# Performance work log

Hardware: AMD Instinct MI355X
Metric: run time of the kernel (lower is better)

Reference implementation:

```python
import jax, jax.numpy as jnp
import numpy as np


def conv3d(x, w, b):
    # x: [B,C,D,H,W], w: [O,I,3,3,3], padding=1, stride=1
    y = jax.lax.conv_general_dilated(
        x, w, window_strides=(1, 1, 1), padding=[(1, 1)] * 3,
        dimension_numbers=("NCDHW", "OIDHW", "NCDHW"))
    return y + b[None, :, None, None, None]


def trilinear_sample(x, cd, ch, cw):
    # x: [B,C,D,H,W]; cd/ch/cw: [B,K,D,H,W] float sampling coords.
    # Zero padding outside the volume (invalid corners masked to 0).
    B, C, D, H, W = x.shape
    d0 = jnp.floor(cd); h0 = jnp.floor(ch); w0 = jnp.floor(cw)
    fd, fh, fw = cd - d0, ch - h0, cw - w0
    d0 = d0.astype(jnp.int32); h0 = h0.astype(jnp.int32); w0 = w0.astype(jnp.int32)
    gather = jax.vmap(lambda xb, z, y, xx: xb[:, z, y, xx])  # -> [B,C,K,D,H,W]
    out = jnp.zeros((B, C) + cd.shape[1:], x.dtype)
    for dz in (0, 1):
        wz = fd if dz else 1.0 - fd
        zi = d0 + dz
        for dy in (0, 1):
            wy = fh if dy else 1.0 - fh
            yi = h0 + dy
            for dx in (0, 1):
                wx = fw if dx else 1.0 - fw
                xi = w0 + dx
                valid = ((zi >= 0) & (zi < D) & (yi >= 0) & (yi < H)
                         & (xi >= 0) & (xi < W)).astype(x.dtype)
                v = gather(x, jnp.clip(zi, 0, D - 1), jnp.clip(yi, 0, H - 1),
                           jnp.clip(xi, 0, W - 1))
                out = out + (wz * wy * wx * valid)[:, None] * v
    return out


def deform_conv3d(x, offsets, mask, w, b):
    # Modulated deformable 3D conv (DCNv2-style), kernel 3x3x3, pad 1, stride 1.
    # offsets: [B,81,D,H,W] = 27 taps x (dd,dh,dw); mask: [B,27,D,H,W].
    B, C, D, H, W = x.shape
    K = 27
    off = offsets.reshape(B, K, 3, D, H, W)
    kd, kh, kw = jnp.meshgrid(jnp.arange(3), jnp.arange(3), jnp.arange(3), indexing="ij")
    tap_d = (kd.reshape(-1) - 1).astype(x.dtype)[None, :, None, None, None]
    tap_h = (kh.reshape(-1) - 1).astype(x.dtype)[None, :, None, None, None]
    tap_w = (kw.reshape(-1) - 1).astype(x.dtype)[None, :, None, None, None]
    gd = jnp.arange(D, dtype=x.dtype)[None, None, :, None, None]
    gh = jnp.arange(H, dtype=x.dtype)[None, None, None, :, None]
    gw = jnp.arange(W, dtype=x.dtype)[None, None, None, None, :]
    cd = gd + tap_d + off[:, :, 0]
    ch = gh + tap_h + off[:, :, 1]
    cw = gw + tap_w + off[:, :, 2]
    sampled = trilinear_sample(x, cd, ch, cw) * mask[:, None]  # [B,C,K,D,H,W]
    out = jnp.einsum("bckdhw,ock->bodhw", sampled, w.reshape(w.shape[0], C, K))
    return out + b[None, :, None, None, None]


def mdconv3d(x, ow, ob, w, b):
    # MDConv3d: internal offset/mask predictor + modulated deformable conv.
    d = conv3d(x, ow, ob)
    offsets, mask = d[:, :81], jax.nn.sigmoid(d[:, 81:])
    return deform_conv3d(x, offsets, mask, w, b)


def forward(x, ow1, ob1, w1, b1, ow2, ob2, w2, b2, ow3, ob3, w3, b3,
            defo_w, defo_b, c3d_w, c3d_b):
    h = jax.nn.relu(mdconv3d(x, ow1, ob1, w1, b1))
    h = jax.nn.relu(mdconv3d(h, ow2, ob2, w2, b2))
    h = jax.nn.relu(mdconv3d(h, ow3, ob3, w3, b3))
    d = conv3d(h, defo_w, defo_b)
    offsets, alpha = d[:, :81], jax.nn.sigmoid(d[:, 81:])
    return deform_conv3d(x, offsets, alpha, c3d_w, c3d_b)


def setup_inputs() -> dict:
    key = jax.random.key(0)
    ks = jax.random.split(key, 16)
    B, C, D, H, W = 1, 256, 8, 32, 32
    M = 256  # mdim
    OFF_SCALE = 0.02  # small init so predicted offsets stay moderate

    def p(k, shape):
        return jax.random.normal(k, shape, jnp.float32) * OFF_SCALE

    inp = {"x": jax.random.normal(ks[0], (B, C, D, H, W), jnp.float32)}
    c_ins = [C, M, M]
    for i, cin in enumerate(c_ins, 1):
        inp[f"ow{i}"] = p(ks[2 * i - 1], (108, cin, 3, 3, 3))
        inp[f"ob{i}"] = jnp.zeros((108,), jnp.float32)
        inp[f"w{i}"] = p(ks[2 * i], (M, cin, 3, 3, 3))
        inp[f"b{i}"] = jnp.zeros((M,), jnp.float32)
    inp["defo_w"] = p(ks[13], (108, M, 3, 3, 3))
    inp["defo_b"] = jnp.zeros((108,), jnp.float32)
    inp["c3d_w"] = p(ks[14], (256, C, 3, 3, 3))
    inp["c3d_b"] = jnp.zeros((256,), jnp.float32)
    return inp


def reference(x, ow1, ob1, w1, b1, ow2, ob2, w2, b2, ow3, ob3, w3, b3,
              defo_w, defo_b, c3d_w, c3d_b):
    return forward(x, ow1, ob1, w1, b1, ow2, ob2, w2, b2, ow3, ob3, w3, b3,
                   defo_w, defo_b, c3d_w, c3d_b)
```

## Files before the change

### kernel.cpp

```cpp
#include <hip/hip_runtime.h>
#include <cstdint>

#define NPOS 8192
#define KTOT 6912
#define XP_ROWS 11560
#define XP_SY 34
#define XP_SZ 1156
#define KS 8
#define KSL 864

typedef float  facc_t __attribute__((ext_vector_type(4)));
typedef short  bf8_t  __attribute__((ext_vector_type(8)));
typedef unsigned short ub8_t __attribute__((ext_vector_type(8)));
typedef float  f4_t   __attribute__((ext_vector_type(4)));

__device__ __forceinline__ unsigned short f2bf(float f) {
    unsigned u = __float_as_uint(f);
    u = (u + 0x7FFFu + ((u >> 16) & 1u)) >> 16;
    return (unsigned short)u;
}
__device__ __forceinline__ float bf2f(unsigned short u) {
    return __uint_as_float(((unsigned)u) << 16);
}

__device__ __forceinline__ void gl_lds16(const unsigned short* g, unsigned short* l) {
    __builtin_amdgcn_global_load_lds(
        (const __attribute__((address_space(1))) unsigned int*)g,
        (__attribute__((address_space(3))) unsigned int*)l, 16, 0, 0);
}

__global__ __launch_bounds__(256) void zero_k(unsigned short* __restrict__ dst) {
    ub8_t zz = {0,0,0,0,0,0,0,0};
    *(ub8_t*)&dst[((size_t)blockIdx.x * 256 + threadIdx.x) * 8] = zz;
}

__global__ __launch_bounds__(256) void pad_x_t(const float* __restrict__ x,
                                               unsigned short* __restrict__ XpA) {
    __shared__ unsigned short T[256 * 33];
    int b = blockIdx.x;
    int z = b >> 5, y = b & 31;
    int t = threadIdx.x;
    int c8 = t >> 5, xv = t & 31;
#pragma unroll 4
    for (int i = 0; i < 32; ++i) {
        int c = i * 8 + c8;
        T[c * 33 + xv] = f2bf(x[c * NPOS + (z << 10) + (y << 5) + xv]);
    }
    __syncthreads();
    int rowb = ((z + 1) * XP_SZ + (y + 1) * XP_SY + 1) * 256;
#pragma unroll 4
    for (int j = 0; j < 32; ++j) {
        XpA[rowb + j * 256 + t] = T[t * 33 + j];
    }
}

__global__ __launch_bounds__(256) void wtrans_all(
    const float* __restrict__ o1, const float* __restrict__ o2,
    const float* __restrict__ o3, const float* __restrict__ o4,
    const float* __restrict__ m1, const float* __restrict__ m2,
    const float* __restrict__ m3, const float* __restrict__ m4,
    unsigned short* __restrict__ wtoff, unsigned short* __restrict__ wtmain) {
    __shared__ float T[6912];
    int b = blockIdx.x, t = threadIdx.x;
    const float* src; unsigned short* dst; int o, O;
    if (b < 512) {
        int L = b >> 7; o = b & 127; O = 108;
        src = (L == 0) ? o1 : (L == 1) ? o2 : (L == 2) ? o3 : o4;
        dst = wtoff + ((size_t)(L * 128 + o)) * KTOT;
    } else {
        int b2 = b - 512;
        int L = b2 >> 8; o = b2 & 255; O = 256;
        src = (L == 0) ? m1 : (L == 1) ? m2 : (L == 2) ? m3 : m4;
        dst = wtmain + ((size_t)(L * 256 + o)) * KTOT;
    }
    if (o < O) {
#pragma unroll 3
        for (int i = 0; i < 27; ++i) T[i * 256 + t] = src[(size_t)o * KTOT + i * 256 + t];
        __syncthreads();
#pragma unroll 3
        for (int i = 0; i < 27; ++i) {
            int kc = i * 256 + t;
            int c = kc & 255, k = kc >> 8;
            dst[kc] = f2bf(T[c * 27 + k]);
        }
    } else {
#pragma unroll 3
        for (int i = 0; i < 27; ++i) dst[i * 256 + t] = 0;
    }
}

template<bool DEFORM>
__global__ __launch_bounds__(256, 4)
void fgemm(const unsigned short* __restrict__ Xp,
           const unsigned short* __restrict__ wt,
           const float* __restrict__ dbuf,
           float* __restrict__ parts) {
    constexpr int O   = DEFORM ? 256 : 128;
    constexpr int PWN = DEFORM ? 4 : 2;
    constexpr int NCH = KSL / 32;
    __shared__ unsigned short Cbuf[DEFORM ? 16384 : 1] __attribute__((aligned(16)));
    __shared__ unsigned short Bs[64 * 32] __attribute__((aligned(16)));
    __shared__ int   rowtab_s[DEFORM ? 64 : 1];
    __shared__ float cwtab_s[DEFORM ? 512 : 1];

    const int t = threadIdx.x;
    const int wave = t >> 6, lane = t & 63;
    const int q = lane >> 4, r = lane & 15;
    const int pbase = blockIdx.x * 64;
    const int ks = blockIdx.y;
    const int kstart = ks * KSL;

    const int obw = DEFORM ? (wave * 64) : ((wave >> 1) * 64);
    const int pfb = DEFORM ? 0 : ((wave & 1) * 32);

    const int pl = t >> 2;
    const int cg = t & 3;
    const int p = pbase + pl;
    const int z = p >> 10, y = (p >> 5) & 31, xx = p & 31;
    const int bswr = pl * 32 + ((cg ^ (pl & 3)) << 3);

    const int sj   = (t >> 2) & 7;
    const int squad = t & 3;
    const int sroff = ((sj >> 2) & 1) * XP_SZ + ((sj >> 1) & 1) * XP_SY + (sj & 1);
    const int sphi = t >> 5;

    facc_t acc[4][PWN];
#pragma unroll
    for (int i = 0; i < 4; ++i)
#pragma unroll
        for (int ip = 0; ip < PWN; ++ip) acc[i][ip] = (facc_t){0.f, 0.f, 0.f, 0.f};

    for (int chunk = 0; chunk < NCH; ++chunk) {
        const int kc0 = kstart + chunk * 32;
        const int k = kc0 >> 8;
        const int c0 = kc0 & 255;

        if (DEFORM) {
            if (chunk == 0 || c0 == 0) {
                if (t < 64) {
                    const int kd = k / 9, kh = (k / 3) % 3, kw = k % 3;
                    int pp = pbase + t;
                    int zz2 = pp >> 10, yy2 = (pp >> 5) & 31, xx2 = pp & 31;
                    float od  = dbuf[(3 * k + 0) * NPOS + pp];
                    float oh  = dbuf[(3 * k + 1) * NPOS + pp];
                    float ow_ = dbuf[(3 * k + 2) * NPOS + pp];
                    float m   = dbuf[(81 + k) * NPOS + pp];
                    float cd = (float)(zz2 + kd - 1) + od;
                    float ch = (float)(yy2 + kh - 1) + oh;
                    float cx = (float)(xx2 + kw - 1) + ow_;
                    float fdf = floorf(cd), fhf = floorf(ch), fwf = floorf(cx);
                    float fd = cd - fdf, fh = ch - fhf, fw = cx - fwf;
                    float wz0 = 1.f - fd, wz1 = fd;
                    float wy0 = 1.f - fh, wy1 = fh;
                    float wx0 = 1.f - fw, wx1 = fw;
                    int id, ih, iw;
                    if (fdf < -1.f || fdf >= 8.f)  { wz0 = 0.f; wz1 = 0.f; id = 0; } else id = (int)fdf;
                    if (fhf < -1.f || fhf >= 32.f) { wy0 = 0.f; wy1 = 0.f; ih = 0; } else ih = (int)fhf;
                    if (fwf < -1.f || fwf >= 32.f) { wx0 = 0.f; wx1 = 0.f; iw = 0; } else iw = (int)fwf;
                    wz0 *= m; wz1 *= m;
                    float w00 = wz0 * wy0, w01 = wz0 * wy1, w10 = wz1 * wy0, w11 = wz1 * wy1;
                    rowtab_s[t] = (id + 1) * XP_SZ + (ih + 1) * XP_SY + (iw + 1);
                    cwtab_s[t * 8 + 0] = w00 * wx0; cwtab_s[t * 8 + 1] = w00 * wx1;
                    cwtab_s[t * 8 + 2] = w01 * wx0; cwtab_s[t * 8 + 3] = w01 * wx1;
                    cwtab_s[t * 8 + 4] = w10 * wx0; cwtab_s[t * 8 + 5] = w10 * wx1;
                    cwtab_s[t * 8 + 6] = w11 * wx0; cwtab_s[t * 8 + 7] = w11 * wx1;
                }
                __syncthreads();
            }
#pragma unroll
            for (int i = 0; i < 8; ++i) {
                int plo = i * 8 + sphi;
                int row = rowtab_s[plo] + sroff;
                gl_lds16(Xp + (size_t)row * 256 + c0 + squad * 8,
                         &Cbuf[(i * 256 + (t & ~63)) * 8]);
            }
            __syncthreads();
            {
                f4_t cw0 = *(const f4_t*)&cwtab_s[pl * 8];
                f4_t cw1 = *(const f4_t*)&cwtab_s[pl * 8 + 4];
                float av[8];
#pragma unroll
                for (int e = 0; e < 8; ++e) av[e] = 0.f;
#pragma unroll
                for (int j = 0; j < 8; ++j) {
                    ub8_t v = *(const ub8_t*)&Cbuf[pl * 256 + j * 32 + cg * 8];
                    float w = (j < 4) ? cw0[j] : cw1[j - 4];
#pragma unroll
                    for (int e = 0; e < 8; ++e) av[e] += w * bf2f(v[e]);
                }
                ub8_t pk;
#pragma unroll
                for (int e = 0; e < 8; ++e) pk[e] = f2bf(av[e]);
                *(ub8_t*)&Bs[bswr] = pk;
            }
        } else {
            const int kd = k / 9, kh = (k / 3) % 3, kw = k % 3;
            int row = (z + kd) * XP_SZ + (y + kh) * XP_SY + (xx + kw);
            ub8_t v = *(const ub8_t*)&Xp[(size_t)row * 256 + c0 + cg * 8];
            *(ub8_t*)&Bs[bswr] = v;
        }
        __syncthreads();

#pragma unroll
        for (int i = 0; i < 4; ++i) {
            bf8_t a = *(const bf8_t*)&wt[(size_t)(obw + i * 16 + r) * KTOT + kc0 + q * 8];
#pragma unroll
            for (int ip = 0; ip < PWN; ++ip) {
                int brow = pfb + ip * 16 + r;
                bf8_t b = *(const bf8_t*)&Bs[brow * 32 + ((q ^ (brow & 3)) << 3)];
                acc[i][ip] = __builtin_amdgcn_mfma_f32_16x16x32_bf16(a, b, acc[i][ip], 0, 0, 0);
            }
        }
        __syncthreads();
    }

    float* pp = parts + (size_t)ks * O * NPOS;
#pragma unroll
    for (int i = 0; i < 4; ++i)
#pragma unroll
        for (int ip = 0; ip < PWN; ++ip)
#pragma unroll
            for (int reg = 0; reg < 4; ++reg) {
                int o = obw + i * 16 + q * 4 + reg;
                int px = pbase + pfb + ip * 16 + r;
                pp[(size_t)o * NPOS + px] = acc[i][ip][reg];
            }
}

__global__ __launch_bounds__(256) void ccombine(const float* __restrict__ parts,
                                                const float* __restrict__ ob,
                                                float* __restrict__ dbuf) {
    int b = blockIdx.x;
    int o = b >> 3;
    int p4 = ((b & 7) * 256 + threadIdx.x) * 4;
    float s0 = 0, s1 = 0, s2 = 0, s3 = 0;
#pragma unroll
    for (int s = 0; s < KS; ++s) {
        const float4 v = *(const float4*)&parts[((size_t)(s * 128 + o)) * NPOS + p4];
        s0 += v.x; s1 += v.y; s2 += v.z; s3 += v.w;
    }
    float bv = ob[o];
    s0 += bv; s1 += bv; s2 += bv; s3 += bv;
    if (o >= 81) {
        s0 = 1.f / (1.f + __expf(-s0));
        s1 = 1.f / (1.f + __expf(-s1));
        s2 = 1.f / (1.f + __expf(-s2));
        s3 = 1.f / (1.f + __expf(-s3));
    }
    *(float4*)&dbuf[(size_t)o * NPOS + p4] = make_float4(s0, s1, s2, s3);
}

__global__ __launch_bounds__(256) void dcombine_h(const float* __restrict__ parts,
                                                  const float* __restrict__ bias,
                                                  unsigned short* __restrict__ XpB) {
    __shared__ unsigned short T[64 * 66];
    int p0 = blockIdx.x * 64, o0 = blockIdx.y * 64;
    int t = threadIdx.x;
    int pl = t & 63, og = t >> 6;
#pragma unroll 4
    for (int j = 0; j < 16; ++j) {
        int ol = og * 16 + j;
        float s = 0.f;
#pragma unroll
        for (int sp = 0; sp < KS; ++sp)
            s += parts[((size_t)(sp * 256 + o0 + ol)) * NPOS + p0 + pl];
        s += bias[o0 + ol];
        T[ol * 66 + pl] = f2bf(fmaxf(s, 0.f));
    }
    __syncthreads();
    int c = t & 63, pr = t >> 6;
#pragma unroll 4
    for (int j = 0; j < 16; ++j) {
        int pl2 = j * 4 + pr;
        int pg = p0 + pl2;
        int zz = pg >> 10, yy = (pg >> 5) & 31, xv = pg & 31;
        int row = (zz + 1) * XP_SZ + (yy + 1) * XP_SY + xv + 1;
        XpB[(size_t)row * 256 + o0 + c] = T[c * 66 + pl2];
    }
}

__global__ __launch_bounds__(256) void dcombine_out(const float* __restrict__ parts,
                                                    const float* __restrict__ bias,
                                                    float* __restrict__ out) {
    int b = blockIdx.x;
    int o = b >> 3;
    int p4 = ((b & 7) * 256 + threadIdx.x) * 4;
    float s0 = 0, s1 = 0, s2 = 0, s3 = 0;
#pragma unroll
    for (int s = 0; s < KS; ++s) {
        const float4 v = *(const float4*)&parts[((size_t)(s * 256 + o)) * NPOS + p4];
        s0 += v.x; s1 += v.y; s2 += v.z; s3 += v.w;
    }
    float bv = bias[o];
    *(float4*)&out[(size_t)o * NPOS + p4] = make_float4(s0 + bv, s1 + bv, s2 + bv, s3 + bv);
}

extern "C" void kernel_launch(void* const* d_in, const int* in_sizes, int n_in,
                              void* d_out, int out_size, void* d_ws, size_t ws_size,
                              hipStream_t stream) {
    const float* x      = (const float*)d_in[0];
    const float* ow1    = (const float*)d_in[1];
    const float* ob1    = (const float*)d_in[2];
    const float* w1     = (const float*)d_in[3];
    const float* b1     = (const float*)d_in[4];
    const float* ow2    = (const float*)d_in[5];
    const float* ob2    = (const float*)d_in[6];
    const float* w2     = (const float*)d_in[7];
    const float* b2     = (const float*)d_in[8];
    const float* ow3    = (const float*)d_in[9];
    const float* ob3    = (const float*)d_in[10];
    const float* w3     = (const float*)d_in[11];
    const float* b3     = (const float*)d_in[12];
    const float* defo_w = (const float*)d_in[13];
    const float* defo_b = (const float*)d_in[14];
    const float* c3d_w  = (const float*)d_in[15];
    const float* c3d_b  = (const float*)d_in[16];
    float* out = (float*)d_out;

    unsigned short* XpA    = (unsigned short*)d_ws;
    unsigned short* XpB    = XpA + (size_t)XP_ROWS * 256;
    unsigned short* wtoff  = XpB + (size_t)XP_ROWS * 256;
    unsigned short* wtmain = wtoff + (size_t)4 * 128 * KTOT;
    float* dbufp = (float*)(wtmain + (size_t)4 * 256 * KTOT);
    float* parts = dbufp + (size_t)108 * NPOS;

    const dim3 blk(256);
    const dim3 gG(128, KS);

    zero_k<<<2890, blk, 0, stream>>>(XpA);
    pad_x_t<<<256, blk, 0, stream>>>(x, XpA);
    wtrans_all<<<1536, blk, 0, stream>>>(ow1, ow2, ow3, defo_w, w1, w2, w3, c3d_w, wtoff, wtmain);

    const float* cbias[4] = {ob1, ob2, ob3, defo_b};
    const float* dbias[4] = {b1, b2, b3, c3d_b};

    for (int L = 0; L < 4; ++L) {
        const unsigned short* featConv = (L == 0) ? XpA : XpB;
        const unsigned short* featDef  = (L == 3) ? XpA : featConv;
        fgemm<false><<<gG, blk, 0, stream>>>(featConv, wtoff + (size_t)L * 128 * KTOT, nullptr, parts);
        ccombine<<<864, blk, 0, stream>>>(parts, cbias[L], dbufp);
        fgemm<true><<<gG, blk, 0, stream>>>(featDef, wtmain + (size_t)L * 256 * KTOT, dbufp, parts);
        if (L < 3) dcombine_h<<<dim3(128, 4), blk, 0, stream>>>(parts, dbias[L], XpB);
        else       dcombine_out<<<2048, blk, 0, stream>>>(parts, dbias[L], out);
    }
}
```

Baseline: 862.1 us.

## Precompute all tap tables up front and prefetch next gather during MFMA

The deformable GEMM kernel now computes the bilinear row/weight tables for every tap in its K-slice once at kernel start, instead of recomputing them with an extra barrier at each tap boundary. The gather of the next chunk into LDS is issued before the current chunk's MFMAs so global latency overlaps compute. The LDS gather layout is also rotated to reduce bank conflicts. The K-split drops from 8 to 6 and the occupancy hint from 4 to 3 blocks, which cuts partial-sum traffic but uses more LDS and leaves fewer resident blocks.

```diff
diff --git a/kernel.cpp b/kernel.cpp
--- a/kernel.cpp
+++ b/kernel.cpp
@@ -6,8 +6,9 @@
 #define XP_ROWS 11560
 #define XP_SY 34
 #define XP_SZ 1156
-#define KS 8
-#define KSL 864
+#define KS 6
+#define KSL 1152
+#define NTAPS 6
 
 typedef float  facc_t __attribute__((ext_vector_type(4)));
 typedef short  bf8_t  __attribute__((ext_vector_type(8)));
@@ -90,7 +91,7 @@
 }
 
 template<bool DEFORM>
-__global__ __launch_bounds__(256, 4)
+__global__ __launch_bounds__(256, 3)
 void fgemm(const unsigned short* __restrict__ Xp,
            const unsigned short* __restrict__ wt,
            const float* __restrict__ dbuf,
@@ -100,8 +101,8 @@
     constexpr int NCH = KSL / 32;
     __shared__ unsigned short Cbuf[DEFORM ? 16384 : 1] __attribute__((aligned(16)));
     __shared__ unsigned short Bs[64 * 32] __attribute__((aligned(16)));
-    __shared__ int   rowtab_s[DEFORM ? 64 : 1];
-    __shared__ float cwtab_s[DEFORM ? 512 : 1];
+    __shared__ int   rowtab[DEFORM ? (NTAPS * 64) : 1];
+    __shared__ float cwtab[DEFORM ? (NTAPS * 512) : 1];
 
     const int t = threadIdx.x;
     const int wave = t >> 6, lane = t & 63;
@@ -109,6 +110,7 @@
     const int pbase = blockIdx.x * 64;
     const int ks = blockIdx.y;
     const int kstart = ks * KSL;
+    const int k0 = kstart >> 8;
 
     const int obw = DEFORM ? (wave * 64) : ((wave >> 1) * 64);
     const int pfb = DEFORM ? 0 : ((wave & 1) * 32);
@@ -119,10 +121,11 @@
     const int z = p >> 10, y = (p >> 5) & 31, xx = p & 31;
     const int bswr = pl * 32 + ((cg ^ (pl & 3)) << 3);
 
-    const int sj   = (t >> 2) & 7;
+    const int sphi  = t >> 5;
+    const int sfld  = (t >> 2) & 7;
+    const int sj    = (sfld - sphi) & 7;
     const int squad = t & 3;
     const int sroff = ((sj >> 2) & 1) * XP_SZ + ((sj >> 1) & 1) * XP_SY + (sj & 1);
-    const int sphi = t >> 5;
 
     facc_t acc[4][PWN];
 #pragma unroll
@@ -130,60 +133,67 @@
 #pragma unroll
         for (int ip = 0; ip < PWN; ++ip) acc[i][ip] = (facc_t){0.f, 0.f, 0.f, 0.f};
 
-    for (int chunk = 0; chunk < NCH; ++chunk) {
-        const int kc0 = kstart + chunk * 32;
-        const int k = kc0 >> 8;
-        const int c0 = kc0 & 255;
-
-        if (DEFORM) {
-            if (chunk == 0 || c0 == 0) {
-                if (t < 64) {
-                    const int kd = k / 9, kh = (k / 3) % 3, kw = k % 3;
-                    int pp = pbase + t;
-                    int zz2 = pp >> 10, yy2 = (pp >> 5) & 31, xx2 = pp & 31;
-                    float od  = dbuf[(3 * k + 0) * NPOS + pp];
-                    float oh  = dbuf[(3 * k + 1) * NPOS + pp];
-                    float ow_ = dbuf[(3 * k + 2) * NPOS + pp];
-                    float m   = dbuf[(81 + k) * NPOS + pp];
-                    float cd = (float)(zz2 + kd - 1) + od;
-                    float ch = (float)(yy2 + kh - 1) + oh;
-                    float cx = (float)(xx2 + kw - 1) + ow_;
-                    float fdf = floorf(cd), fhf = floorf(ch), fwf = floorf(cx);
-                    float fd = cd - fdf, fh = ch - fhf, fw = cx - fwf;
-                    float wz0 = 1.f - fd, wz1 = fd;
-                    float wy0 = 1.f - fh, wy1 = fh;
-                    float wx0 = 1.f - fw, wx1 = fw;
-                    int id, ih, iw;
-                    if (fdf < -1.f || fdf >= 8.f)  { wz0 = 0.f; wz1 = 0.f; id = 0; } else id = (int)fdf;
-                    if (fhf < -1.f || fhf >= 32.f) { wy0 = 0.f; wy1 = 0.f; ih = 0; } else ih = (int)fhf;
-                    if (fwf < -1.f || fwf >= 32.f) { wx0 = 0.f; wx1 = 0.f; iw = 0; } else iw = (int)fwf;
-                    wz0 *= m; wz1 *= m;
-                    float w00 = wz0 * wy0, w01 = wz0 * wy1, w10 = wz1 * wy0, w11 = wz1 * wy1;
-                    rowtab_s[t] = (id + 1) * XP_SZ + (ih + 1) * XP_SY + (iw + 1);
-                    cwtab_s[t * 8 + 0] = w00 * wx0; cwtab_s[t * 8 + 1] = w00 * wx1;
-                    cwtab_s[t * 8 + 2] = w01 * wx0; cwtab_s[t * 8 + 3] = w01 * wx1;
-                    cwtab_s[t * 8 + 4] = w10 * wx0; cwtab_s[t * 8 + 5] = w10 * wx1;
-                    cwtab_s[t * 8 + 6] = w11 * wx0; cwtab_s[t * 8 + 7] = w11 * wx1;
-                }
-                __syncthreads();
-            }
+    if (DEFORM) {
+        const int ntaps = ((kstart + KSL - 1) >> 8) - k0 + 1;
+        for (int it = t; it < ntaps * 64; it += 256) {
+            int s = it >> 6;
+            int k = k0 + s;
+            int pp = pbase + (it & 63);
+            int zz2 = pp >> 10, yy2 = (pp >> 5) & 31, xx2 = pp & 31;
+            const int kd = k / 9, kh = (k / 3) % 3, kw = k % 3;
+            float od  = dbuf[(3 * k + 0) * NPOS + pp];
+            float oh  = dbuf[(3 * k + 1) * NPOS + pp];
+            float ow_ = dbuf[(3 * k + 2) * NPOS + pp];
+            float m   = dbuf[(81 + k) * NPOS + pp];
+            float cd = (float)(zz2 + kd - 1) + od;
+            float ch = (float)(yy2 + kh - 1) + oh;
+            float cx = (float)(xx2 + kw - 1) + ow_;
+            float fdf = floorf(cd), fhf = floorf(ch), fwf = floorf(cx);
+            float fd = cd - fdf, fh = ch - fhf, fw = cx - fwf;
+            float wz0 = 1.f - fd, wz1 = fd;
+            float wy0 = 1.f - fh, wy1 = fh;
+            float wx0 = 1.f - fw, wx1 = fw;
+            int id, ih, iw;
+            if (fdf < -1.f || fdf >= 8.f)  { wz0 = 0.f; wz1 = 0.f; id = 0; } else id = (int)fdf;
+            if (fhf < -1.f || fhf >= 32.f) { wy0 = 0.f; wy1 = 0.f; ih = 0; } else ih = (int)fhf;
+            if (fwf < -1.f || fwf >= 32.f) { wx0 = 0.f; wx1 = 0.f; iw = 0; } else iw = (int)fwf;
+            wz0 *= m; wz1 *= m;
+            float w00 = wz0 * wy0, w01 = wz0 * wy1, w10 = wz1 * wy0, w11 = wz1 * wy1;
+            rowtab[it] = (id + 1) * XP_SZ + (ih + 1) * XP_SY + (iw + 1);
+            cwtab[it * 8 + 0] = w00 * wx0; cwtab[it * 8 + 1] = w00 * wx1;
+            cwtab[it * 8 + 2] = w01 * wx0; cwtab[it * 8 + 3] = w01 * wx1;
+            cwtab[it * 8 + 4] = w10 * wx0; cwtab[it * 8 + 5] = w10 * wx1;
+            cwtab[it * 8 + 6] = w11 * wx0; cwtab[it * 8 + 7] = w11 * wx1;
+        }
+        __syncthreads();
+
+        {
+            const int c0 = kstart & 255;
+            const int ts0 = 0;
 #pragma unroll
             for (int i = 0; i < 8; ++i) {
-                int plo = i * 8 + sphi;
-                int row = rowtab_s[plo] + sroff;
+                int row = rowtab[ts0 * 64 + i * 8 + sphi] + sroff;
                 gl_lds16(Xp + (size_t)row * 256 + c0 + squad * 8,
                          &Cbuf[(i * 256 + (t & ~63)) * 8]);
             }
-            __syncthreads();
+        }
+        __syncthreads();
+
+        for (int n = 0; n < NCH; ++n) {
+            const int kc0 = kstart + n * 32;
+            const int tslot = (kc0 >> 8) - k0;
             {
-                f4_t cw0 = *(const f4_t*)&cwtab_s[pl * 8];
-                f4_t cw1 = *(const f4_t*)&cwtab_s[pl * 8 + 4];
+                const float* cwp = &cwtab[(tslot * 64 + pl) * 8];
+                f4_t cw0 = *(const f4_t*)cwp;
+                f4_t cw1 = *(const f4_t*)(cwp + 4);
                 float av[8];
 #pragma unroll
                 for (int e = 0; e < 8; ++e) av[e] = 0.f;
+                const int sbase = (pl >> 3) * 256 + (pl & 7) * 32 + cg;
 #pragma unroll
                 for (int j = 0; j < 8; ++j) {
-                    ub8_t v = *(const ub8_t*)&Cbuf[pl * 256 + j * 32 + cg * 8];
+                    int f = (j + (pl & 7)) & 7;
+                    ub8_t v = *(const ub8_t*)&Cbuf[(sbase + f * 4) * 8];
                     float w = (j < 4) ? cw0[j] : cw1[j - 4];
 #pragma unroll
                     for (int e = 0; e < 8; ++e) av[e] += w * bf2f(v[e]);
@@ -193,25 +203,53 @@
                 for (int e = 0; e < 8; ++e) pk[e] = f2bf(av[e]);
                 *(ub8_t*)&Bs[bswr] = pk;
             }
-        } else {
+            __syncthreads();
+
+            if (n + 1 < NCH) {
+                const int kc1 = kstart + (n + 1) * 32;
+                const int c1 = kc1 & 255;
+                const int ts1 = (kc1 >> 8) - k0;
+#pragma unroll
+                for (int i = 0; i < 8; ++i) {
+                    int row = rowtab[ts1 * 64 + i * 8 + sphi] + sroff;
+                    gl_lds16(Xp + (size_t)row * 256 + c1 + squad * 8,
+                             &Cbuf[(i * 256 + (t & ~63)) * 8]);
+                }
+            }
+#pragma unroll
+            for (int i = 0; i < 4; ++i) {
+                bf8_t a = *(const bf8_t*)&wt[(size_t)(obw + i * 16 + r) * KTOT + kc0 + q * 8];
+#pragma unroll
+                for (int ip = 0; ip < PWN; ++ip) {
+                    int brow = ip * 16 + r;
+                    bf8_t b = *(const bf8_t*)&Bs[brow * 32 + ((q ^ (brow & 3)) << 3)];
+                    acc[i][ip] = __builtin_amdgcn_mfma_f32_16x16x32_bf16(a, b, acc[i][ip], 0, 0, 0);
+                }
+            }
+            __syncthreads();
+        }
+    } else {
+        for (int n = 0; n < NCH; ++n) {
+            const int kc0 = kstart + n * 32;
+            const int k = kc0 >> 8;
+            const int c0 = kc0 & 255;
             const int kd = k / 9, kh = (k / 3) % 3, kw = k % 3;
             int row = (z + kd) * XP_SZ + (y + kh) * XP_SY + (xx + kw);
             ub8_t v = *(const ub8_t*)&Xp[(size_t)row * 256 + c0 + cg * 8];
             *(ub8_t*)&Bs[bswr] = v;
-        }
-        __syncthreads();
-
-#pragma unroll
-        for (int i = 0; i < 4; ++i) {
-            bf8_t a = *(const bf8_t*)&wt[(size_t)(obw + i * 16 + r) * KTOT + kc0 + q * 8];
-#pragma unroll
-            for (int ip = 0; ip < PWN; ++ip) {
-                int brow = pfb + ip * 16 + r;
-                bf8_t b = *(const bf8_t*)&Bs[brow * 32 + ((q ^ (brow & 3)) << 3)];
-                acc[i][ip] = __builtin_amdgcn_mfma_f32_16x16x32_bf16(a, b, acc[i][ip], 0, 0, 0);
-            }
-        }
-        __syncthreads();
+            __syncthreads();
+#pragma unroll
+            for (int i = 0; i < 4; ++i) {
+                bf8_t a = *(const bf8_t*)&wt[(size_t)(obw + i * 16 + r) * KTOT + kc0 + q * 8];
+#pragma unroll
+                for (int ip = 0; ip < PWN; ++ip) {
+                    int brow = pfb + ip * 16 + r;
+                    bf8_t b = *(const bf8_t*)&Bs[brow * 32 + ((q ^ (brow & 3)) << 3)];
+                    acc[i][ip] = __builtin_amdgcn_mfma_f32_16x16x32_bf16(a, b, acc[i][ip], 0, 0, 0);
+                }
+            }
+            __syncthreads();
+        }
     }
 
     float* pp = parts + (size_t)ks * O * NPOS;
```

Result: faster. 835.2 us (-3.1%).
